# Optimization experiments

Measured on AMD Instinct MI355X. Metric: run time of the kernel, lower is better.

The kernel has to match this reference:

```python
import jax, jax.numpy as jnp
import numpy as np

N, H, VOCAB = 512, 512, 32000

def setup_inputs() -> dict:
    key = jax.random.key(0)
    ks = jax.random.split(key, 7)
    s1 = 1.0 / np.sqrt(N)
    s2 = 1.0 / np.sqrt(H)
    return {
        "r_l": jax.random.normal(ks[0], (4, 256, N), dtype=jnp.float32),
        "W1": jax.random.uniform(ks[1], (H, N), jnp.float32, -s1, s1),
        "b1": jax.random.uniform(ks[2], (H,), jnp.float32, -s1, s1),
        "W2": jax.random.uniform(ks[3], (H * N, H), jnp.float32, -s2, s2),
        "b2": jax.random.uniform(ks[4], (H * N,), jnp.float32, -s2, s2),
        "W_out": jax.random.uniform(ks[5], (VOCAB, H), jnp.float32, -s2, s2),
        "b_out": jax.random.uniform(ks[6], (VOCAB,), jnp.float32, -s2, s2),
    }

def reference(r_l, W1, b1, W2, b2, W_out, b_out):
    B, L, n = r_l.shape
    r = r_l.reshape(B * L, n)                      # (T, N)
    x = jax.nn.relu(r @ W1.T + b1)                 # (T, H)
    W_att = (x @ W2.T + b2).reshape(-1, H, N)      # (T, H, N) per-token weights
    r_ol = jnp.einsum('thn,tn->th', W_att, r)      # batched GEMV
    logits = r_ol @ W_out.T + b_out                # (T, vocab)
    return logits.reshape(B, L, VOCAB)
```

## Files before the change

kernel.cpp:

```cpp
#include <hip/hip_runtime.h>
#include <hip/hip_bf16.h>

typedef __attribute__((ext_vector_type(8))) short short8;
typedef __attribute__((ext_vector_type(4))) short short4v;
typedef __attribute__((ext_vector_type(4))) float floatx4;

static __device__ __forceinline__ unsigned short f2bf(float f){
  union { float f; unsigned int u; } v; v.f = f;
  return (unsigned short)((v.u + 0x7FFFu + ((v.u >> 16) & 1u)) >> 16);
}
static __device__ __forceinline__ float bf2f(unsigned short b){
  union { unsigned int u; float f; } v; v.u = ((unsigned int)b) << 16; return v.f;
}
static __device__ __forceinline__ short8 cvt8_pk(floatx4 a, floatx4 b){
  union { __hip_bfloat162 h[4]; short8 s; } u;
  u.h[0] = __float22bfloat162_rn(float2{a[0], a[1]});
  u.h[1] = __float22bfloat162_rn(float2{a[2], a[3]});
  u.h[2] = __float22bfloat162_rn(float2{b[0], b[1]});
  u.h[3] = __float22bfloat162_rn(float2{b[2], b[3]});
  return u.s;
}
static __device__ __forceinline__ short4v cvt4(floatx4 a){
  union { __hip_bfloat162 h[2]; short4v s; } u;
  u.h[0] = __float22bfloat162_rn(float2{a[0], a[1]});
  u.h[1] = __float22bfloat162_rn(float2{a[2], a[3]});
  return u.s;
}
static __device__ __forceinline__ short8 frag_ld(const char* ldsbase, int row, int kbyte){
  return *(const short8*)(ldsbase + row*256 + (kbyte ^ ((row & 15) << 4)));
}
static __device__ __forceinline__ short8 frag_ld64(const char* base, int row, int kbyte){
  return *(const short8*)(base + row*128 + (kbyte ^ ((row & 7) << 4)));
}

template<int ROWS>
static __device__ __forceinline__ void stage_tile(char* ldsbase, const float* __restrict__ src,
                                                  int ld, int tid){
  #pragma unroll
  for (int w = 0; w < ROWS/32; ++w){
    int g = w*512 + tid;
    int row = g >> 4, k8 = g & 15;
    const float* p = src + (size_t)row*ld + k8*8;
    floatx4 v0 = *(const floatx4*)p;
    floatx4 v1 = *(const floatx4*)(p+4);
    *(short8*)(ldsbase + row*256 + ((k8*16) ^ ((row & 15) << 4))) = cvt8_pk(v0, v1);
  }
}

template<int MODE>
__global__ __launch_bounds__(512)
void gemm_plain(const float* __restrict__ Asrc, const float* __restrict__ Bsrc,
                const float* __restrict__ bias, void* __restrict__ out, int out_ld){
  __shared__ char smem[98304];
  char* At = smem;
  char* Bt = smem + 65536;
  const int tid  = threadIdx.x;
  const int lane = tid & 63, w = tid >> 6;
  const int wm = w & 3, wn = w >> 2;
  const int bid = blockIdx.x;
  const int t0 = (bid & 3) * 256;
  const int c0 = (bid >> 2) * 128;
  const int rbase = wm*64, cbase = wn*64;

  floatx4 acc[4][4];
  #pragma unroll
  for (int i=0;i<4;++i)
    #pragma unroll
    for (int j=0;j<4;++j) acc[i][j] = floatx4{0.f,0.f,0.f,0.f};

  for (int kb = 0; kb < 4; ++kb){
    __syncthreads();
    stage_tile<256>(At, Asrc + (size_t)t0*512 + kb*128, 512, tid);
    stage_tile<128>(Bt, Bsrc + (size_t)c0*512 + kb*128, 512, tid);
    __syncthreads();
    #pragma unroll
    for (int ks = 0; ks < 4; ++ks){
      const int kbyte = (ks*32 + (lane>>4)*8) * 2;
      short8 af[4], bfr[4];
      #pragma unroll
      for (int mi=0; mi<4; ++mi) af[mi] = frag_ld(At, rbase + mi*16 + (lane&15), kbyte);
      #pragma unroll
      for (int ni=0; ni<4; ++ni) bfr[ni] = frag_ld(Bt, cbase + ni*16 + (lane&15), kbyte);
      #pragma unroll
      for (int mi=0; mi<4; ++mi)
        #pragma unroll
        for (int ni=0; ni<4; ++ni)
          acc[mi][ni] = __builtin_amdgcn_mfma_f32_16x16x32_bf16(af[mi], bfr[ni], acc[mi][ni], 0,0,0);
    }
  }
  #pragma unroll
  for (int mi=0; mi<4; ++mi){
    #pragma unroll
    for (int ni=0; ni<4; ++ni){
      #pragma unroll
      for (int rg=0; rg<4; ++rg){
        int t = t0 + rbase + mi*16 + (lane>>4)*4 + rg;
        int c = c0 + cbase + ni*16 + (lane&15);
        float v = acc[mi][ni][rg];
        if (MODE == 0){
          v += bias[c]; v = v > 0.f ? v : 0.f;
          ((unsigned short*)out)[(size_t)t*out_ld + c] = f2bf(v);
        } else {
          ((float*)out)[(size_t)t*out_ld + c] = v;
        }
      }
    }
  }
}

__attribute__((amdgpu_waves_per_eu(2, 2)))
__global__ __launch_bounds__(512)
void k2_fold(const unsigned short* __restrict__ xbf, const float* __restrict__ r,
             const float* __restrict__ W2, float* __restrict__ r_ol){
  __shared__ char smem[147456];
  unsigned short* RT2 = (unsigned short*)(smem + 131072);
  const int tid  = threadIdx.x;
  const int lane = tid & 63, w = tid >> 6;
  const int wm = w & 3, wn = w >> 2;
  const int bid = blockIdx.x;
  const int xr = bid & 7, idx = bid >> 3;
  const int m  = idx & 3, gh = idx >> 2;
  const int g  = xr + 8*gh;
  const int ht = g & 3, ns = g >> 2;
  const int t0 = m*256, h0 = ht*128, n0 = ns*32;

  #pragma unroll
  for (int i = 0; i < 16; ++i){
    int e = i*512 + tid; int row = e >> 5, c = e & 31;
    RT2[c*256 + row] = f2bf(r[(size_t)(t0+row)*512 + n0 + c]);
  }

  floatx4 acc[4][4];
  #pragma unroll
  for (int i=0;i<4;++i)
    #pragma unroll
    for (int j=0;j<4;++j) acc[i][j] = floatx4{0.f,0.f,0.f,0.f};

  floatx4 lb[8];
  short8 af[4][4];

  auto stageA = [&](int kb2){
    const int chunk = tid & 15, rbase_ = tid >> 4;
    #pragma unroll
    for (int j = 0; j < 8; ++j){
      const int row = rbase_ + j*32;
      short8 v = *(const short8*)(xbf + (size_t)(t0+row)*512 + kb2*128 + chunk*8);
      *(short8*)(smem + row*256 + (((chunk ^ (row & 15)) << 4))) = v;
    }
  };
  auto issueB = [&](int n, int kb2){
    const int c16 = tid & 31, rb = tid >> 5;
    const float* base = W2 + (size_t)(n0+n)*512 + (size_t)kb2*128 + c16*4;
    #pragma unroll
    for (int j = 0; j < 8; ++j)
      lb[j] = *(const floatx4*)(base + (size_t)(h0 + rb + j*16)*262144);
  };
  auto cvtB = [&](char* Bb){
    const int c8 = tid & 31, rb = tid >> 5;
    #pragma unroll
    for (int j = 0; j < 8; ++j){
      const int row = rb + j*16;
      const int byte = (((c8 >> 1) ^ (row & 15)) << 4) | ((c8 & 1) << 3);
      *(short4v*)(Bb + row*256 + byte) = cvt4(lb[j]);
    }
  };
  auto loadA = [&](){
    #pragma unroll
    for (int ks = 0; ks < 4; ++ks){
      const int kbyte = ks*64 + (lane>>4)*16;
      #pragma unroll
      for (int mi = 0; mi < 4; ++mi)
        af[ks][mi] = frag_ld(smem, wm*64 + mi*16 + (lane&15), kbyte);
    }
  };
  auto compute_fold = [&](const char* Bb, int n){
    float rvv[4][4];
    #pragma unroll
    for (int mi = 0; mi < 4; ++mi){
      const int rrow = wm*64 + mi*16 + (lane>>4)*4;
      short4v tv = *(const short4v*)(RT2 + n*256 + rrow);
      #pragma unroll
      for (int j = 0; j < 4; ++j) rvv[mi][j] = bf2f((unsigned short)tv[j]);
    }
    #pragma unroll
    for (int half = 0; half < 2; ++half){
      floatx4 ct[4][2];
      #pragma unroll
      for (int ks = 0; ks < 4; ++ks){
        const int kbyte = ks*64 + (lane>>4)*16;
        short8 bfr[2];
        #pragma unroll
        for (int nh = 0; nh < 2; ++nh)
          bfr[nh] = frag_ld(Bb, wn*64 + (half*2+nh)*16 + (lane&15), kbyte);
        __builtin_amdgcn_s_setprio(1);
        #pragma unroll
        for (int mi = 0; mi < 4; ++mi)
          #pragma unroll
          for (int nh = 0; nh < 2; ++nh)
            ct[mi][nh] = __builtin_amdgcn_mfma_f32_16x16x32_bf16(
                af[ks][mi], bfr[nh], (ks==0) ? floatx4{0.f,0.f,0.f,0.f} : ct[mi][nh], 0,0,0);
        __builtin_amdgcn_s_setprio(0);
      }
      #pragma unroll
      for (int mi = 0; mi < 4; ++mi)
        #pragma unroll
        for (int nh = 0; nh < 2; ++nh){
          acc[mi][half*2+nh][0] += rvv[mi][0] * ct[mi][nh][0];
          acc[mi][half*2+nh][1] += rvv[mi][1] * ct[mi][nh][1];
          acc[mi][half*2+nh][2] += rvv[mi][2] * ct[mi][nh][2];
          acc[mi][half*2+nh][3] += rvv[mi][3] * ct[mi][nh][3];
        }
    }
  };

  stageA(0);
  issueB(0, 0);
  cvtB(smem + 65536);
  __syncthreads();

  int cur = 0;
  for (int kb2 = 0; kb2 < 4; ++kb2){
    loadA();
    for (int n = 0; n < 32; ++n){
      const int bi = kb2*32 + n;
      if (bi < 127){
        const int nn = (n == 31) ? 0 : n + 1;
        const int nk = (n == 31) ? kb2 + 1 : kb2;
        issueB(nn, nk);
      }
      compute_fold(smem + 65536 + cur*32768, n);
      if (bi < 127) cvtB(smem + 65536 + (cur^1)*32768);
      __syncthreads();
      cur ^= 1;
    }
    if (kb2 < 3){
      stageA(kb2 + 1);
      __syncthreads();
    }
  }

  #pragma unroll
  for (int ni = 0; ni < 4; ++ni){
    const int h = h0 + wn*64 + ni*16 + (lane & 15);
    #pragma unroll
    for (int mi = 0; mi < 4; ++mi){
      #pragma unroll
      for (int rg = 0; rg < 4; ++rg){
        const int t = t0 + wm*64 + mi*16 + (lane >> 4)*4 + rg;
        atomicAdd(&r_ol[(size_t)t*512 + h], acc[mi][ni][rg]);
      }
    }
  }
}

__global__ __launch_bounds__(512, 2)
void gemm_out(const float* __restrict__ Asrc, const float* __restrict__ Bsrc,
              const float* __restrict__ bias, float* __restrict__ out){
  __shared__ char smem[98304];
  const int tid  = threadIdx.x;
  const int lane = tid & 63, w = tid >> 6;
  const int wm = w & 3, wn = w >> 2;
  const int bid = blockIdx.x;
  const int t0 = (bid & 3) * 256;
  const int c0 = (bid >> 2) * 128;

  floatx4 acc[4][4];
  #pragma unroll
  for (int i=0;i<4;++i)
    #pragma unroll
    for (int j=0;j<4;++j) acc[i][j] = floatx4{0.f,0.f,0.f,0.f};

  floatx4 la[8], lb[4];
  const int r16 = tid >> 4, c4 = tid & 15;

  auto issue = [&](int s){
    const int K0 = s*64;
    #pragma unroll
    for (int it=0; it<8; ++it){
      int row = it*32 + r16;
      la[it] = *(const floatx4*)(Asrc + (size_t)(t0+row)*512 + K0 + c4*4);
    }
    #pragma unroll
    for (int it=0; it<4; ++it){
      int row = it*32 + r16;
      lb[it] = *(const floatx4*)(Bsrc + (size_t)(c0+row)*512 + K0 + c4*4);
    }
  };
  auto write_buf = [&](int buf){
    char* ad = smem + buf*32768;
    #pragma unroll
    for (int it=0; it<8; ++it){
      int row = it*32 + r16;
      *(short4v*)(ad + row*128 + ((c4*8) ^ ((row & 7) << 4))) = cvt4(la[it]);
    }
    char* bd = smem + 65536 + buf*16384;
    #pragma unroll
    for (int it=0; it<4; ++it){
      int row = it*32 + r16;
      *(short4v*)(bd + row*128 + ((c4*8) ^ ((row & 7) << 4))) = cvt4(lb[it]);
    }
  };
  auto compute = [&](int buf){
    const char* Ab = smem + buf*32768;
    const char* Bb = smem + 65536 + buf*16384;
    #pragma unroll
    for (int ks = 0; ks < 2; ++ks){
      const int kbyte = ks*64 + (lane >> 4)*16;
      short8 af[4], bfr[4];
      #pragma unroll
      for (int mi = 0; mi < 4; ++mi) af[mi] = frag_ld64(Ab, wm*64 + mi*16 + (lane&15), kbyte);
      #pragma unroll
      for (int ni = 0; ni < 4; ++ni) bfr[ni] = frag_ld64(Bb, wn*64 + ni*16 + (lane&15), kbyte);
      __builtin_amdgcn_s_setprio(1);
      #pragma unroll
      for (int mi = 0; mi < 4; ++mi)
        #pragma unroll
        for (int ni = 0; ni < 4; ++ni)
          acc[mi][ni] = __builtin_amdgcn_mfma_f32_16x16x32_bf16(af[mi], bfr[ni], acc[mi][ni], 0,0,0);
      __builtin_amdgcn_s_setprio(0);
    }
  };

  issue(0);
  write_buf(0);
  __syncthreads();
  for (int s = 0; s < 8; ++s){
    const int cur = s & 1;
    if (s < 7) issue(s + 1);
    compute(cur);
    if (s < 7){
      write_buf(cur ^ 1);
      __syncthreads();
    }
  }

  #pragma unroll
  for (int ni = 0; ni < 4; ++ni){
    const int c = c0 + wn*64 + ni*16 + (lane & 15);
    const float bv = bias[c];
    #pragma unroll
    for (int mi = 0; mi < 4; ++mi){
      #pragma unroll
      for (int rg = 0; rg < 4; ++rg){
        const int t = t0 + wm*64 + mi*16 + (lane >> 4)*4 + rg;
        out[(size_t)t*32000 + c] = acc[mi][ni][rg] + bv;
      }
    }
  }
}

extern "C" void kernel_launch(void* const* d_in, const int* in_sizes, int n_in,
                              void* d_out, int out_size, void* d_ws, size_t ws_size,
                              hipStream_t stream) {
  const float* r    = (const float*)d_in[0];
  const float* W1   = (const float*)d_in[1];
  const float* b1   = (const float*)d_in[2];
  const float* W2   = (const float*)d_in[3];
  const float* b2   = (const float*)d_in[4];
  const float* Wout = (const float*)d_in[5];
  const float* bout = (const float*)d_in[6];
  float* logits = (float*)d_out;

  unsigned short* x_bf = (unsigned short*)d_ws;
  float* r_ol = (float*)((char*)d_ws + 1024*512*2);

  gemm_plain<0><<<16, 512, 0, stream>>>(r, W1, b1, x_bf, 512);
  gemm_plain<1><<<16, 512, 0, stream>>>(r, b2, nullptr, r_ol, 512);
  k2_fold<<<256, 512, 0, stream>>>(x_bf, r, W2, r_ol);
  gemm_out<<<1000, 512, 0, stream>>>(r_ol, Wout, bout, logits);
}
```

Baseline: 409.1 us.

## Halve k2_fold token tile, load A fragments from global, split B staging

The fold kernel's token tile shrinks from 256 to 128 rows and the grid doubles to 512 blocks. Shared memory drops from 144KB to 72KB, so more blocks can be resident per CU. The x operand is no longer staged in shared memory: each wave now reads its A fragments straight from global memory, which removes the stageA barriers. W2 loads now read contiguous 8-float segments per thread and are split into two halves interleaved with the two MFMA halves to hide latency. The trade-off is that each W2 tile is fetched and converted twice as often in total, since every block reuses it over half as many tokens.

```diff
diff --git a/kernel.cpp b/kernel.cpp
--- a/kernel.cpp
+++ b/kernel.cpp
@@ -108,145 +108,160 @@
   }
 }
 
-__attribute__((amdgpu_waves_per_eu(2, 2)))
 __global__ __launch_bounds__(512)
 void k2_fold(const unsigned short* __restrict__ xbf, const float* __restrict__ r,
              const float* __restrict__ W2, float* __restrict__ r_ol){
-  __shared__ char smem[147456];
-  unsigned short* RT2 = (unsigned short*)(smem + 131072);
+  __shared__ char smem[73728];
+  unsigned short* RT2 = (unsigned short*)(smem + 65536);
   const int tid  = threadIdx.x;
   const int lane = tid & 63, w = tid >> 6;
   const int wm = w & 3, wn = w >> 2;
   const int bid = blockIdx.x;
   const int xr = bid & 7, idx = bid >> 3;
-  const int m  = idx & 3, gh = idx >> 2;
-  const int g  = xr + 8*gh;
+  const int m = idx & 7, slot = idx >> 3;
+  const int g = xr + 8*slot;
   const int ht = g & 3, ns = g >> 2;
-  const int t0 = m*256, h0 = ht*128, n0 = ns*32;
-
-  #pragma unroll
-  for (int i = 0; i < 16; ++i){
+  const int t0 = m*128, h0 = ht*128, n0 = ns*32;
+
+  #pragma unroll
+  for (int i = 0; i < 8; ++i){
     int e = i*512 + tid; int row = e >> 5, c = e & 31;
-    RT2[c*256 + row] = f2bf(r[(size_t)(t0+row)*512 + n0 + c]);
-  }
-
-  floatx4 acc[4][4];
-  #pragma unroll
-  for (int i=0;i<4;++i)
+    RT2[c*128 + row] = f2bf(r[(size_t)(t0+row)*512 + n0 + c]);
+  }
+
+  floatx4 acc[2][4];
+  #pragma unroll
+  for (int i=0;i<2;++i)
     #pragma unroll
     for (int j=0;j<4;++j) acc[i][j] = floatx4{0.f,0.f,0.f,0.f};
 
-  floatx4 lb[8];
-  short8 af[4][4];
-
-  auto stageA = [&](int kb2){
-    const int chunk = tid & 15, rbase_ = tid >> 4;
-    #pragma unroll
-    for (int j = 0; j < 8; ++j){
-      const int row = rbase_ + j*32;
-      short8 v = *(const short8*)(xbf + (size_t)(t0+row)*512 + kb2*128 + chunk*8);
-      *(short8*)(smem + row*256 + (((chunk ^ (row & 15)) << 4))) = v;
-    }
-  };
-  auto issueB = [&](int n, int kb2){
-    const int c16 = tid & 31, rb = tid >> 5;
-    const float* base = W2 + (size_t)(n0+n)*512 + (size_t)kb2*128 + c16*4;
-    #pragma unroll
-    for (int j = 0; j < 8; ++j)
-      lb[j] = *(const floatx4*)(base + (size_t)(h0 + rb + j*16)*262144);
-  };
-  auto cvtB = [&](char* Bb){
-    const int c8 = tid & 31, rb = tid >> 5;
-    #pragma unroll
-    for (int j = 0; j < 8; ++j){
-      const int row = rb + j*16;
-      const int byte = (((c8 >> 1) ^ (row & 15)) << 4) | ((c8 & 1) << 3);
-      *(short4v*)(Bb + row*256 + byte) = cvt4(lb[j]);
-    }
-  };
-  auto loadA = [&](){
-    #pragma unroll
-    for (int ks = 0; ks < 4; ++ks){
-      const int kbyte = ks*64 + (lane>>4)*16;
-      #pragma unroll
-      for (int mi = 0; mi < 4; ++mi)
-        af[ks][mi] = frag_ld(smem, wm*64 + mi*16 + (lane&15), kbyte);
-    }
-  };
-  auto compute_fold = [&](const char* Bb, int n){
-    float rvv[4][4];
-    #pragma unroll
-    for (int mi = 0; mi < 4; ++mi){
-      const int rrow = wm*64 + mi*16 + (lane>>4)*4;
-      short4v tv = *(const short4v*)(RT2 + n*256 + rrow);
-      #pragma unroll
-      for (int j = 0; j < 4; ++j) rvv[mi][j] = bf2f((unsigned short)tv[j]);
-    }
-    #pragma unroll
-    for (int half = 0; half < 2; ++half){
-      floatx4 ct[4][2];
-      #pragma unroll
-      for (int ks = 0; ks < 4; ++ks){
-        const int kbyte = ks*64 + (lane>>4)*16;
-        short8 bfr[2];
-        #pragma unroll
-        for (int nh = 0; nh < 2; ++nh)
-          bfr[nh] = frag_ld(Bb, wn*64 + (half*2+nh)*16 + (lane&15), kbyte);
-        __builtin_amdgcn_s_setprio(1);
-        #pragma unroll
-        for (int mi = 0; mi < 4; ++mi)
-          #pragma unroll
-          for (int nh = 0; nh < 2; ++nh)
-            ct[mi][nh] = __builtin_amdgcn_mfma_f32_16x16x32_bf16(
-                af[ks][mi], bfr[nh], (ks==0) ? floatx4{0.f,0.f,0.f,0.f} : ct[mi][nh], 0,0,0);
-        __builtin_amdgcn_s_setprio(0);
-      }
-      #pragma unroll
-      for (int mi = 0; mi < 4; ++mi)
-        #pragma unroll
-        for (int nh = 0; nh < 2; ++nh){
-          acc[mi][half*2+nh][0] += rvv[mi][0] * ct[mi][nh][0];
-          acc[mi][half*2+nh][1] += rvv[mi][1] * ct[mi][nh][1];
-          acc[mi][half*2+nh][2] += rvv[mi][2] * ct[mi][nh][2];
-          acc[mi][half*2+nh][3] += rvv[mi][3] * ct[mi][nh][3];
-        }
-    }
-  };
-
-  stageA(0);
-  issueB(0, 0);
-  cvtB(smem + 65536);
+  floatx4 lb[4];
+  short8 af[4][2];
+
+  const int seg16 = tid & 15, rb = tid >> 4;
+
+  auto loadA = [&](int kb2){
+    #pragma unroll
+    for (int ks = 0; ks < 4; ++ks)
+      #pragma unroll
+      for (int mi = 0; mi < 2; ++mi)
+        af[ks][mi] = *(const short8*)(xbf
+            + (size_t)(t0 + wm*32 + mi*16 + (lane&15))*512
+            + kb2*128 + ks*32 + (lane>>4)*8);
+  };
+  auto issueB = [&](int n, int kb2, int hf){
+    #pragma unroll
+    for (int j = 0; j < 2; ++j){
+      const int row = rb + (hf*2 + j)*32;
+      const float* p = W2 + (size_t)(h0+row)*262144 + (size_t)(n0+n)*512 + kb2*128 + seg16*8;
+      lb[j*2]   = *(const floatx4*)p;
+      lb[j*2+1] = *(const floatx4*)(p+4);
+    }
+  };
+  auto cvtB = [&](char* Bb, int hf){
+    #pragma unroll
+    for (int j = 0; j < 2; ++j){
+      const int row = rb + (hf*2 + j)*32;
+      *(short8*)(Bb + row*256 + ((seg16 ^ (row & 15)) << 4)) = cvt8_pk(lb[j*2], lb[j*2+1]);
+    }
+  };
+
+  issueB(0, 0, 0); cvtB(smem, 0);
+  issueB(0, 0, 1); cvtB(smem, 1);
   __syncthreads();
 
   int cur = 0;
   for (int kb2 = 0; kb2 < 4; ++kb2){
-    loadA();
+    loadA(kb2);
     for (int n = 0; n < 32; ++n){
       const int bi = kb2*32 + n;
-      if (bi < 127){
-        const int nn = (n == 31) ? 0 : n + 1;
-        const int nk = (n == 31) ? kb2 + 1 : kb2;
-        issueB(nn, nk);
-      }
-      compute_fold(smem + 65536 + cur*32768, n);
-      if (bi < 127) cvtB(smem + 65536 + (cur^1)*32768);
+      const bool hn = (bi < 127);
+      const int nn = (n == 31) ? 0 : n + 1;
+      const int nk = (n == 31) ? kb2 + 1 : kb2;
+      const char* Bb = smem + cur*32768;
+      char* Bnx = smem + (cur^1)*32768;
+
+      float rvv[2][4];
+      #pragma unroll
+      for (int mi = 0; mi < 2; ++mi){
+        const int rrow = wm*32 + mi*16 + (lane>>4)*4;
+        short4v tv = *(const short4v*)(RT2 + n*128 + rrow);
+        #pragma unroll
+        for (int j = 0; j < 4; ++j) rvv[mi][j] = bf2f((unsigned short)tv[j]);
+      }
+
+      if (hn) issueB(nn, nk, 0);
+      {
+        floatx4 ct[2][2];
+        #pragma unroll
+        for (int ks = 0; ks < 4; ++ks){
+          const int kbyte = ks*64 + (lane>>4)*16;
+          short8 bfr[2];
+          #pragma unroll
+          for (int nh = 0; nh < 2; ++nh)
+            bfr[nh] = frag_ld(Bb, wn*64 + nh*16 + (lane&15), kbyte);
+          __builtin_amdgcn_s_setprio(1);
+          #pragma unroll
+          for (int mi = 0; mi < 2; ++mi)
+            #pragma unroll
+            for (int nh = 0; nh < 2; ++nh)
+              ct[mi][nh] = __builtin_amdgcn_mfma_f32_16x16x32_bf16(
+                  af[ks][mi], bfr[nh], (ks==0) ? floatx4{0.f,0.f,0.f,0.f} : ct[mi][nh], 0,0,0);
+          __builtin_amdgcn_s_setprio(0);
+        }
+        #pragma unroll
+        for (int mi = 0; mi < 2; ++mi)
+          #pragma unroll
+          for (int nh = 0; nh < 2; ++nh){
+            acc[mi][nh][0] += rvv[mi][0] * ct[mi][nh][0];
+            acc[mi][nh][1] += rvv[mi][1] * ct[mi][nh][1];
+            acc[mi][nh][2] += rvv[mi][2] * ct[mi][nh][2];
+            acc[mi][nh][3] += rvv[mi][3] * ct[mi][nh][3];
+          }
+      }
+      if (hn){ cvtB(Bnx, 0); issueB(nn, nk, 1); }
+      {
+        floatx4 ct[2][2];
+        #pragma unroll
+        for (int ks = 0; ks < 4; ++ks){
+          const int kbyte = ks*64 + (lane>>4)*16;
+          short8 bfr[2];
+          #pragma unroll
+          for (int nh = 0; nh < 2; ++nh)
+            bfr[nh] = frag_ld(Bb, wn*64 + (2+nh)*16 + (lane&15), kbyte);
+          __builtin_amdgcn_s_setprio(1);
+          #pragma unroll
+          for (int mi = 0; mi < 2; ++mi)
+            #pragma unroll
+            for (int nh = 0; nh < 2; ++nh)
+              ct[mi][nh] = __builtin_amdgcn_mfma_f32_16x16x32_bf16(
+                  af[ks][mi], bfr[nh], (ks==0) ? floatx4{0.f,0.f,0.f,0.f} : ct[mi][nh], 0,0,0);
+          __builtin_amdgcn_s_setprio(0);
+        }
+        #pragma unroll
+        for (int mi = 0; mi < 2; ++mi)
+          #pragma unroll
+          for (int nh = 0; nh < 2; ++nh){
+            acc[mi][2+nh][0] += rvv[mi][0] * ct[mi][nh][0];
+            acc[mi][2+nh][1] += rvv[mi][1] * ct[mi][nh][1];
+            acc[mi][2+nh][2] += rvv[mi][2] * ct[mi][nh][2];
+            acc[mi][2+nh][3] += rvv[mi][3] * ct[mi][nh][3];
+          }
+      }
+      if (hn) cvtB(Bnx, 1);
       __syncthreads();
       cur ^= 1;
     }
-    if (kb2 < 3){
-      stageA(kb2 + 1);
-      __syncthreads();
-    }
   }
 
   #pragma unroll
   for (int ni = 0; ni < 4; ++ni){
     const int h = h0 + wn*64 + ni*16 + (lane & 15);
     #pragma unroll
-    for (int mi = 0; mi < 4; ++mi){
+    for (int mi = 0; mi < 2; ++mi){
       #pragma unroll
       for (int rg = 0; rg < 4; ++rg){
-        const int t = t0 + wm*64 + mi*16 + (lane >> 4)*4 + rg;
+        const int t = t0 + wm*32 + mi*16 + (lane >> 4)*4 + rg;
         atomicAdd(&r_ol[(size_t)t*512 + h], acc[mi][ni][rg]);
       }
     }
@@ -366,6 +381,6 @@
 
   gemm_plain<0><<<16, 512, 0, stream>>>(r, W1, b1, x_bf, 512);
   gemm_plain<1><<<16, 512, 0, stream>>>(r, b2, nullptr, r_ol, 512);
-  k2_fold<<<256, 512, 0, stream>>>(x_bf, r, W2, r_ol);
+  k2_fold<<<512, 512, 0, stream>>>(x_bf, r, W2, r_ol);
   gemm_out<<<1000, 512, 0, stream>>>(r_ol, Wout, bout, logits);
 }
```

Result: slower. 539.4 us (+31.9%).

## Interleave B conversion with MFMA phases using split barriers in fold kernel

Applied to the files above, without the earlier changes.

The fold kernel's per-n iteration is restructured into four phases separated by raw s_barrier calls. The bf16 conversion and LDS stores of the next W2 tile are spread across those phases, so they overlap with the MFMA work instead of running after it. The waves_per_eu attribute is dropped, and gemm_out's block-to-tile mapping is changed so consecutive blocks share the same row tile of the A operand. The extra barriers add synchronisation overhead, and correctness now depends on the manual waitcnt placement.

```diff
diff --git a/kernel.cpp b/kernel.cpp
--- a/kernel.cpp
+++ b/kernel.cpp
@@ -108,10 +108,9 @@
   }
 }
 
-__attribute__((amdgpu_waves_per_eu(2, 2)))
 __global__ __launch_bounds__(512)
-void k2_fold(const unsigned short* __restrict__ xbf, const float* __restrict__ r,
-             const float* __restrict__ W2, float* __restrict__ r_ol){
+void k2_fold8(const unsigned short* __restrict__ xbf, const float* __restrict__ r,
+              const float* __restrict__ W2, float* __restrict__ r_ol){
   __shared__ char smem[147456];
   unsigned short* RT2 = (unsigned short*)(smem + 131072);
   const int tid  = threadIdx.x;
@@ -138,6 +137,7 @@
 
   floatx4 lb[8];
   short8 af[4][4];
+  const int c16 = tid & 31, rb = tid >> 5;
 
   auto stageA = [&](int kb2){
     const int chunk = tid & 15, rbase_ = tid >> 4;
@@ -148,74 +148,35 @@
       *(short8*)(smem + row*256 + (((chunk ^ (row & 15)) << 4))) = v;
     }
   };
+  auto loadA = [&](){
+    #pragma unroll
+    for (int ks = 0; ks < 4; ++ks){
+      const int kbyte = ks*64 + (lane>>4)*16;
+      #pragma unroll
+      for (int mi = 0; mi < 4; ++mi)
+        af[ks][mi] = frag_ld(smem, wm*64 + mi*16 + (lane&15), kbyte);
+    }
+  };
   auto issueB = [&](int n, int kb2){
-    const int c16 = tid & 31, rb = tid >> 5;
     const float* base = W2 + (size_t)(n0+n)*512 + (size_t)kb2*128 + c16*4;
     #pragma unroll
     for (int j = 0; j < 8; ++j)
       lb[j] = *(const floatx4*)(base + (size_t)(h0 + rb + j*16)*262144);
   };
-  auto cvtB = [&](char* Bb){
-    const int c8 = tid & 31, rb = tid >> 5;
-    #pragma unroll
-    for (int j = 0; j < 8; ++j){
+  auto cvtChunk = [&](char* Bb, int c){
+    #pragma unroll
+    for (int i = 0; i < 2; ++i){
+      const int j = c*2 + i;
       const int row = rb + j*16;
-      const int byte = (((c8 >> 1) ^ (row & 15)) << 4) | ((c8 & 1) << 3);
+      const int byte = (((c16 >> 1) ^ (row & 15)) << 4) | ((c16 & 1) << 3);
       *(short4v*)(Bb + row*256 + byte) = cvt4(lb[j]);
-    }
-  };
-  auto loadA = [&](){
-    #pragma unroll
-    for (int ks = 0; ks < 4; ++ks){
-      const int kbyte = ks*64 + (lane>>4)*16;
-      #pragma unroll
-      for (int mi = 0; mi < 4; ++mi)
-        af[ks][mi] = frag_ld(smem, wm*64 + mi*16 + (lane&15), kbyte);
-    }
-  };
-  auto compute_fold = [&](const char* Bb, int n){
-    float rvv[4][4];
-    #pragma unroll
-    for (int mi = 0; mi < 4; ++mi){
-      const int rrow = wm*64 + mi*16 + (lane>>4)*4;
-      short4v tv = *(const short4v*)(RT2 + n*256 + rrow);
-      #pragma unroll
-      for (int j = 0; j < 4; ++j) rvv[mi][j] = bf2f((unsigned short)tv[j]);
-    }
-    #pragma unroll
-    for (int half = 0; half < 2; ++half){
-      floatx4 ct[4][2];
-      #pragma unroll
-      for (int ks = 0; ks < 4; ++ks){
-        const int kbyte = ks*64 + (lane>>4)*16;
-        short8 bfr[2];
-        #pragma unroll
-        for (int nh = 0; nh < 2; ++nh)
-          bfr[nh] = frag_ld(Bb, wn*64 + (half*2+nh)*16 + (lane&15), kbyte);
-        __builtin_amdgcn_s_setprio(1);
-        #pragma unroll
-        for (int mi = 0; mi < 4; ++mi)
-          #pragma unroll
-          for (int nh = 0; nh < 2; ++nh)
-            ct[mi][nh] = __builtin_amdgcn_mfma_f32_16x16x32_bf16(
-                af[ks][mi], bfr[nh], (ks==0) ? floatx4{0.f,0.f,0.f,0.f} : ct[mi][nh], 0,0,0);
-        __builtin_amdgcn_s_setprio(0);
-      }
-      #pragma unroll
-      for (int mi = 0; mi < 4; ++mi)
-        #pragma unroll
-        for (int nh = 0; nh < 2; ++nh){
-          acc[mi][half*2+nh][0] += rvv[mi][0] * ct[mi][nh][0];
-          acc[mi][half*2+nh][1] += rvv[mi][1] * ct[mi][nh][1];
-          acc[mi][half*2+nh][2] += rvv[mi][2] * ct[mi][nh][2];
-          acc[mi][half*2+nh][3] += rvv[mi][3] * ct[mi][nh][3];
-        }
     }
   };
 
   stageA(0);
   issueB(0, 0);
-  cvtB(smem + 65536);
+  #pragma unroll
+  for (int c = 0; c < 4; ++c) cvtChunk(smem + 65536, c);
   __syncthreads();
 
   int cur = 0;
@@ -223,19 +184,75 @@
     loadA();
     for (int n = 0; n < 32; ++n){
       const int bi = kb2*32 + n;
-      if (bi < 127){
-        const int nn = (n == 31) ? 0 : n + 1;
-        const int nk = (n == 31) ? kb2 + 1 : kb2;
-        issueB(nn, nk);
-      }
-      compute_fold(smem + 65536 + cur*32768, n);
-      if (bi < 127) cvtB(smem + 65536 + (cur^1)*32768);
-      __syncthreads();
+      const bool hn = (bi < 127);
+      const int nn = (n == 31) ? 0 : n + 1;
+      const int nk = (n == 31) ? kb2 + 1 : kb2;
+      const char* Bc = smem + 65536 + cur*32768;
+      char* Bn = smem + 65536 + (cur^1)*32768;
+
+      float rvv[4][4];
+      #pragma unroll
+      for (int mi = 0; mi < 4; ++mi){
+        const int rrow = wm*64 + mi*16 + (lane>>4)*4;
+        short4v tv = *(const short4v*)(RT2 + n*256 + rrow);
+        #pragma unroll
+        for (int j = 0; j < 4; ++j) rvv[mi][j] = bf2f((unsigned short)tv[j]);
+      }
+      if (hn) issueB(nn, nk);
+
+      floatx4 ct[4][2];
+      #pragma unroll
+      for (int q = 0; q < 2; ++q){
+        #pragma unroll
+        for (int kh = 0; kh < 2; ++kh){
+          if (q == 1 && kh == 0 && hn) cvtChunk(Bn, 2);
+          if (q == 1 && kh == 1 && hn) cvtChunk(Bn, 3);
+          if (q == 0 && kh == 1 && hn){ cvtChunk(Bn, 0); cvtChunk(Bn, 1); }
+          short8 bfr[2][2];
+          #pragma unroll
+          for (int ks2 = 0; ks2 < 2; ++ks2){
+            const int kbyte = (kh*2 + ks2)*64 + (lane>>4)*16;
+            #pragma unroll
+            for (int nh = 0; nh < 2; ++nh)
+              bfr[ks2][nh] = frag_ld(Bc, wn*64 + (q*2+nh)*16 + (lane&15), kbyte);
+          }
+          __builtin_amdgcn_s_barrier();
+          __builtin_amdgcn_s_setprio(1);
+          #pragma unroll
+          for (int ks2 = 0; ks2 < 2; ++ks2){
+            const int ks = kh*2 + ks2;
+            #pragma unroll
+            for (int mi = 0; mi < 4; ++mi)
+              #pragma unroll
+              for (int nh = 0; nh < 2; ++nh)
+                ct[mi][nh] = __builtin_amdgcn_mfma_f32_16x16x32_bf16(
+                    af[ks][mi], bfr[ks2][nh],
+                    (kh==0 && ks2==0) ? floatx4{0.f,0.f,0.f,0.f} : ct[mi][nh], 0,0,0);
+          }
+          __builtin_amdgcn_s_setprio(0);
+          if (kh == 1){
+            #pragma unroll
+            for (int mi = 0; mi < 4; ++mi)
+              #pragma unroll
+              for (int nh = 0; nh < 2; ++nh){
+                acc[mi][q*2+nh][0] += rvv[mi][0] * ct[mi][nh][0];
+                acc[mi][q*2+nh][1] += rvv[mi][1] * ct[mi][nh][1];
+                acc[mi][q*2+nh][2] += rvv[mi][2] * ct[mi][nh][2];
+                acc[mi][q*2+nh][3] += rvv[mi][3] * ct[mi][nh][3];
+              }
+          }
+          if (q == 1 && kh == 1){
+            asm volatile("s_waitcnt lgkmcnt(0)" ::: "memory");
+          }
+          __builtin_amdgcn_s_barrier();
+        }
+      }
       cur ^= 1;
     }
     if (kb2 < 3){
       stageA(kb2 + 1);
-      __syncthreads();
+      asm volatile("s_waitcnt lgkmcnt(0)" ::: "memory");
+      __builtin_amdgcn_s_barrier();
     }
   }
 
@@ -261,8 +278,8 @@
   const int lane = tid & 63, w = tid >> 6;
   const int wm = w & 3, wn = w >> 2;
   const int bid = blockIdx.x;
-  const int t0 = (bid & 3) * 256;
-  const int c0 = (bid >> 2) * 128;
+  const int t0 = (bid / 250) * 256;
+  const int c0 = (bid % 250) * 128;
 
   floatx4 acc[4][4];
   #pragma unroll
@@ -366,6 +383,6 @@
 
   gemm_plain<0><<<16, 512, 0, stream>>>(r, W1, b1, x_bf, 512);
   gemm_plain<1><<<16, 512, 0, stream>>>(r, b2, nullptr, r_ol, 512);
-  k2_fold<<<256, 512, 0, stream>>>(x_bf, r, W2, r_ol);
+  k2_fold8<<<256, 512, 0, stream>>>(x_bf, r, W2, r_ol);
   gemm_out<<<1000, 512, 0, stream>>>(r_ol, Wout, bout, logits);
 }
```

Result: slower. 515.1 us (+25.9%).
